# Performance work log

Hardware: AMD Instinct MI355X
Metric: run time of the kernel (lower is better)

Reference implementation:

```python
import jax, jax.numpy as jnp
import numpy as np

B, L, DIM = 2, 2048, 1024
H, DH, W = 16, 64, 256  # heads, head_dim, window_size
ROPE_BASE = 10000.0


def _rope(x):
    # x: [b, l, h, d] -> rotate consecutive pairs (torch view_as_complex semantics)
    l, d = x.shape[1], x.shape[3]
    freqs = 1.0 / (ROPE_BASE ** (jnp.arange(0, d, 2, dtype=jnp.float32) / d))  # [d/2]
    ang = jnp.arange(l, dtype=jnp.float32)[:, None] * freqs[None, :]           # [l, d/2]
    cos = jnp.cos(ang)[None, :, None, :].astype(x.dtype)
    sin = jnp.sin(ang)[None, :, None, :].astype(x.dtype)
    xe, xo = x[..., 0::2], x[..., 1::2]
    ye = xe * cos - xo * sin
    yo = xe * sin + xo * cos
    return jnp.stack([ye, yo], axis=-1).reshape(x.shape)


def setup_inputs() -> dict:
    key = jax.random.key(0)
    ks = jax.random.split(key, 7)
    sh = (B, L, DIM)
    return {
        "q": jax.random.normal(ks[0], sh, jnp.float32),
        "k": jax.random.normal(ks[1], sh, jnp.float32),
        "v": jax.random.normal(ks[2], sh, jnp.float32),
        "wq": jax.random.normal(ks[3], (H * DH, DIM), jnp.float32) * 0.02,
        "wk": jax.random.normal(ks[4], (H * DH, DIM), jnp.float32) * 0.02,
        "wv": jax.random.normal(ks[5], (H * DH, DIM), jnp.float32) * 0.02,
        "wo": jax.random.normal(ks[6], (DIM, H * DH), jnp.float32) * 0.02,
    }


def reference(q, k, v, wq, wk, wv, wo):
    b, l, _ = q.shape
    qh = (q @ wq.T).reshape(b, l, H, DH)
    kh = (k @ wk.T).reshape(b, l, H, DH)
    vh = (v @ wv.T).reshape(b, l, H, DH).transpose(0, 2, 1, 3)  # [b,h,l,d]
    qh = _rope(qh).transpose(0, 2, 1, 3)                        # [b,h,l,d]
    kh = _rope(kh).transpose(0, 2, 1, 3)
    scores = jnp.einsum('bhqd,bhkd->bhqk', qh, kh) * (DH ** -0.5)
    i = jnp.arange(l)[:, None]
    j = jnp.arange(l)[None, :]
    window_mask = (j <= i) & (j >= i - W)  # keys in [i-W, i], matches the loop
    scores = jnp.where(window_mask, scores, -1e30)
    probs = jax.nn.softmax(scores, axis=-1)
    out = jnp.einsum('bhqk,bhkd->bhqd', probs, vh)
    out = out.transpose(0, 2, 1, 3).reshape(b, l, H * DH)
    return out @ wo.T
```

## Files before the change

kernel.cpp:

```cpp
#include <hip/hip_runtime.h>
#include <stdint.h>

#define B_    2
#define L_    2048
#define DIM_  1024
#define H_    16
#define DH_   64
#define WWIN  256

typedef __attribute__((ext_vector_type(4))) float f32x4;
typedef __attribute__((ext_vector_type(8))) short bf16x8;

__device__ __forceinline__ unsigned short f2bf(float x) {
  union { float f; unsigned u; } c; c.f = x;
  unsigned r = c.u + 0x7fffu + ((c.u >> 16) & 1u);
  return (unsigned short)(r >> 16);
}

struct CastArgs {
  const float* src[7];
  unsigned short* dst[7];
  int n[7];
};
__global__ __launch_bounds__(256) void cast_bf16_kernel(CastArgs a) {
  int arr = blockIdx.y;
  int i = (blockIdx.x * 256 + threadIdx.x) * 4;
  if (i >= a.n[arr]) return;
  float4 v = *(const float4*)(a.src[arr] + i);
  ushort4 o;
  o.x = f2bf(v.x); o.y = f2bf(v.y); o.z = f2bf(v.z); o.w = f2bf(v.w);
  *(ushort4*)(a.dst[arr] + i) = o;
}

#define BM 128
#define BN 64
#define BK 64

__device__ __forceinline__ void gld_lds16(const void* g, void* l) {
  __builtin_amdgcn_global_load_lds(
      (const __attribute__((address_space(1))) void*)g,
      (__attribute__((address_space(3))) void*)l, 16, 0, 0);
}

__device__ __forceinline__ void gemm_core_1024(
    const unsigned short* __restrict__ A, const unsigned short* __restrict__ Bt,
    unsigned short* As, unsigned short* Bs, f32x4 (&acc)[2][4],
    int m0, int n0) {
  const int tid = threadIdx.x;
  const int wave = tid >> 6, lane = tid & 63;
  const int quad = lane >> 4, l16 = lane & 15;
  const int srow = tid >> 3, sc = tid & 7;

  auto stage = [&](int k0, int buf) {
    unsigned short* Ad = As + buf * 8192;
    unsigned short* Bd = Bs + buf * 4096;
    #pragma unroll
    for (int rd = 0; rd < 4; ++rd) {
      int row = rd * 32 + srow;
      int cs = sc ^ (row & 7);
      gld_lds16(A + (size_t)(m0 + row) * 1024 + k0 + cs * 8, Ad + row * BK + sc * 8);
    }
    #pragma unroll
    for (int rd = 0; rd < 2; ++rd) {
      int row = rd * 32 + srow;
      int cs = sc ^ (row & 7);
      gld_lds16(Bt + (size_t)(n0 + row) * 1024 + k0 + cs * 8, Bd + row * BK + sc * 8);
    }
  };

  stage(0, 0);
  for (int k = 0; k < 16; ++k) {
    const int cur = k & 1;
    __syncthreads();
    if (k < 15) stage((k + 1) * BK, cur ^ 1);
    const unsigned short* Ac = As + cur * 8192;
    const unsigned short* Bc = Bs + cur * 4096;
    #pragma unroll
    for (int ks = 0; ks < 2; ++ks) {
      bf16x8 af[2], bfr[4];
      #pragma unroll
      for (int i = 0; i < 2; ++i) {
        int row = wave * 32 + i * 16 + l16;
        int ch = (ks * 4 + quad) ^ (row & 7);
        af[i] = *(const bf16x8*)(Ac + row * BK + ch * 8);
      }
      #pragma unroll
      for (int j = 0; j < 4; ++j) {
        int row = j * 16 + l16;
        int ch = (ks * 4 + quad) ^ (row & 7);
        bfr[j] = *(const bf16x8*)(Bc + row * BK + ch * 8);
      }
      #pragma unroll
      for (int i = 0; i < 2; ++i)
        #pragma unroll
        for (int j = 0; j < 4; ++j)
          acc[i][j] = __builtin_amdgcn_mfma_f32_16x16x32_bf16(af[i], bfr[j], acc[i][j], 0, 0, 0);
    }
  }
}

struct ProjArgs {
  const unsigned short* A[3];
  const unsigned short* Bt[3];
  unsigned short* C[3];
};
__global__ __launch_bounds__(256) void gemm_proj_kernel(ProjArgs pa) {
  __shared__ unsigned short SH[24576];
  unsigned short* As = SH;
  unsigned short* Bs = SH + 16384;

  const int bflat = blockIdx.x;
  const int xcd = bflat & 7, s = bflat >> 3;
  const int nblk = s & 15;
  const int mz = xcd * 12 + (s >> 4);
  const int z = mz >> 5;
  const int mblk = mz & 31;
  const int m0 = mblk * BM, n0 = nblk * BN;

  f32x4 acc[2][4] = {};
  gemm_core_1024(pa.A[z], pa.Bt[z], As, Bs, acc, m0, n0);

  const int tid = threadIdx.x;
  const int lane = tid & 63, wave = tid >> 6;
  const int quad = lane >> 4, l16 = lane & 15;

  if (z < 2) {
    float frev[4];
    #pragma unroll
    for (int j = 0; j < 4; ++j) {
      int d = j * 16 + l16;
      frev[j] = exp2f(-(float)(d >> 1) * 0.41524101186092029f) * 0.15915494309189535f;
    }
    unsigned short* C = pa.C[z];
    const int h = nblk;
    const bool even = (l16 & 1) == 0;
    #pragma unroll
    for (int i = 0; i < 2; ++i)
      #pragma unroll
      for (int r = 0; r < 4; ++r) {
        int m = m0 + wave * 32 + i * 16 + quad * 4 + r;
        int b = m >> 11, l = m & (L_ - 1);
        float lf = (float)l;
        #pragma unroll
        for (int j = 0; j < 4; ++j) {
          int d = j * 16 + l16;
          float v = acc[i][j][r];
          float p = __shfl_xor(v, 1);
          float a = lf * frev[j];
          float t = a - floorf(a);
          float sn = __builtin_amdgcn_sinf(t);
          float cs = __builtin_amdgcn_cosf(t);
          float o = even ? (v * cs - p * sn) : (p * sn + v * cs);
          C[(((size_t)b * H_ + h) * L_ + l) * DH_ + d] = f2bf(o);
        }
      }
  } else {
    __syncthreads();
    unsigned short* T = SH + wave * 2304;
    #pragma unroll
    for (int i = 0; i < 2; ++i)
      #pragma unroll
      for (int j = 0; j < 4; ++j) {
        int nw = j * 16 + l16;
        int hm = i * 4 + quad;
        uint2 pk;
        pk.x = (unsigned)f2bf(acc[i][j][0]) | ((unsigned)f2bf(acc[i][j][1]) << 16);
        pk.y = (unsigned)f2bf(acc[i][j][2]) | ((unsigned)f2bf(acc[i][j][3]) << 16);
        *(uint2*)(T + nw * 36 + hm * 4) = pk;
      }
    asm volatile("s_waitcnt lgkmcnt(0)" ::: "memory");
    int h = nblk;
    int d = lane;
    int b = m0 >> 11;
    int lbase = (m0 & (L_ - 1)) + wave * 32;
    unsigned short* C = pa.C[2];
    size_t rowbase = (((size_t)b * H_ + h) * DH_ + d) * L_ + lbase;
    #pragma unroll
    for (int t = 0; t < 4; ++t) {
      uint2 lo = *(uint2*)(T + lane * 36 + t * 8);
      uint2 hi = *(uint2*)(T + lane * 36 + t * 8 + 4);
      uint4 o = {lo.x, lo.y, hi.x, hi.y};
      *(uint4*)(C + rowbase + t * 8) = o;
    }
  }
}

__global__ __launch_bounds__(256) void gemm_out_kernel(
    const unsigned short* __restrict__ A, const unsigned short* __restrict__ Bt,
    float* __restrict__ C) {
  __shared__ unsigned short SH[24576];
  unsigned short* As = SH;
  unsigned short* Bs = SH + 16384;

  const int bflat = blockIdx.x;
  const int xcd = bflat & 7, s = bflat >> 3;
  const int nblk = s & 15;
  const int mblk = xcd * 4 + (s >> 4);
  const int m0 = mblk * BM, n0 = nblk * BN;

  f32x4 acc[2][4] = {};
  gemm_core_1024(A, Bt, As, Bs, acc, m0, n0);

  const int lane = threadIdx.x & 63, wave = threadIdx.x >> 6;
  const int quad = lane >> 4, l16 = lane & 15;
  #pragma unroll
  for (int i = 0; i < 2; ++i)
    #pragma unroll
    for (int j = 0; j < 4; ++j)
      #pragma unroll
      for (int r = 0; r < 4; ++r) {
        int m = m0 + wave * 32 + i * 16 + quad * 4 + r;
        int n = n0 + j * 16 + l16;
        C[(size_t)m * DIM_ + n] = acc[i][j][r];
      }
}

#define NCH 20
__global__ __launch_bounds__(256) void attn_kernel(
    const unsigned short* __restrict__ Qh,
    const unsigned short* __restrict__ Kh,
    const unsigned short* __restrict__ Vt,
    unsigned short* __restrict__ O) {
  __shared__ unsigned short KVs[160 * 72];
  __shared__ unsigned short Ps[4][16 * 40];
  const int tid = threadIdx.x;
  const int wave = tid >> 6, lane = tid & 63;
  const int quad = lane >> 4, l16 = lane & 15;

  const int bflat = blockIdx.x;
  const int xcd = bflat & 7, s = bflat >> 3;
  const int qt = s >> 2;
  const int bh = xcd * 4 + (s & 3);

  const int q0 = qt * 64;
  const int kwin0 = q0 - WWIN;
  const int qb = q0 + wave * 16;

  bf16x8 qf0, qf1;
  {
    const unsigned short* qrow = Qh + ((size_t)bh * L_ + qb + l16) * DH_;
    qf0 = *(const bf16x8*)(qrow + quad * 8);
    qf1 = *(const bf16x8*)(qrow + 32 + quad * 8);
  }

  f32x4 S[NCH] = {};

  #pragma unroll
  for (int half = 0; half < 2; ++half) {
    __syncthreads();
    for (int rep = 0; rep < 5; ++rep) {
      int ci = rep * 256 + tid;
      int row = ci >> 3, c = ci & 7;
      int key = kwin0 + half * 160 + row;
      uint4 val = {0, 0, 0, 0};
      if (key >= 0)
        val = *(const uint4*)(Kh + ((size_t)bh * L_ + key) * DH_ + c * 8);
      *(uint4*)(&KVs[row * 72 + c * 8]) = val;
    }
    __syncthreads();
    #pragma unroll
    for (int cc = 0; cc < 10; ++cc) {
      const unsigned short* kr = &KVs[(cc * 16 + l16) * 72];
      bf16x8 kf0 = *(const bf16x8*)(kr + quad * 8);
      bf16x8 kf1 = *(const bf16x8*)(kr + 32 + quad * 8);
      int c = half * 10 + cc;
      S[c] = __builtin_amdgcn_mfma_f32_16x16x32_bf16(qf0, kf0, S[c], 0, 0, 0);
      S[c] = __builtin_amdgcn_mfma_f32_16x16x32_bf16(qf1, kf1, S[c], 0, 0, 0);
    }
  }

  float inv_l[4];
  #pragma unroll
  for (int r = 0; r < 4; ++r) {
    int i = qb + quad * 4 + r;
    float mx = -1e30f;
    #pragma unroll
    for (int c = 0; c < NCH; ++c) {
      int key = kwin0 + c * 16 + l16;
      bool valid = (key >= 0) && (key <= i) && (key >= i - WWIN);
      float v = valid ? S[c][r] * 0.125f : -1e30f;
      S[c][r] = v;
      mx = fmaxf(mx, v);
    }
    mx = fmaxf(mx, __shfl_xor(mx, 1));
    mx = fmaxf(mx, __shfl_xor(mx, 2));
    mx = fmaxf(mx, __shfl_xor(mx, 4));
    mx = fmaxf(mx, __shfl_xor(mx, 8));
    float sum = 0.f;
    #pragma unroll
    for (int c = 0; c < NCH; ++c) {
      float e = __expf(S[c][r] - mx);
      S[c][r] = e;
      sum += e;
    }
    sum += __shfl_xor(sum, 1);
    sum += __shfl_xor(sum, 2);
    sum += __shfl_xor(sum, 4);
    sum += __shfl_xor(sum, 8);
    inv_l[r] = 1.0f / sum;
  }

  f32x4 Oacc[4] = {};
  #pragma unroll
  for (int half = 0; half < 2; ++half) {
    __syncthreads();
    for (int rep = 0; rep < 5; ++rep) {
      int ci = rep * 256 + tid;
      int row = ci / 20, c = ci % 20;
      int key0 = kwin0 + half * 160 + c * 8;
      uint4 val = {0, 0, 0, 0};
      if (key0 >= 0)
        val = *(const uint4*)(Vt + ((size_t)bh * DH_ + row) * L_ + key0);
      *(uint4*)(&KVs[row * 168 + c * 8]) = val;
    }
    __syncthreads();
    #pragma unroll
    for (int s5 = 0; s5 < 5; ++s5) {
      int cbase = half * 10 + s5 * 2;
      unsigned short* pw = &Ps[wave][0];
      #pragma unroll
      for (int cc = 0; cc < 2; ++cc)
        #pragma unroll
        for (int r = 0; r < 4; ++r) {
          float p = S[cbase + cc][r] * inv_l[r];
          pw[(quad * 4 + r) * 40 + cc * 16 + l16] = f2bf(p);
        }
      asm volatile("s_waitcnt lgkmcnt(0)" ::: "memory");
      bf16x8 pf = *(const bf16x8*)(pw + l16 * 40 + quad * 8);
      int lk = s5 * 32 + quad * 8;
      #pragma unroll
      for (int t = 0; t < 4; ++t) {
        bf16x8 vf = *(const bf16x8*)(&KVs[(t * 16 + l16) * 168 + lk]);
        Oacc[t] = __builtin_amdgcn_mfma_f32_16x16x32_bf16(pf, vf, Oacc[t], 0, 0, 0);
      }
    }
  }

  int b = bh >> 4, h = bh & 15;
  #pragma unroll
  for (int t = 0; t < 4; ++t)
    #pragma unroll
    for (int r = 0; r < 4; ++r) {
      int l = qb + quad * 4 + r;
      int col = h * DH_ + t * 16 + l16;
      O[((size_t)b * L_ + l) * (H_ * DH_) + col] = f2bf(Oacc[t][r]);
    }
}

extern "C" void kernel_launch(void* const* d_in, const int* in_sizes, int n_in,
                              void* d_out, int out_size, void* d_ws, size_t ws_size,
                              hipStream_t stream) {
  const float* q  = (const float*)d_in[0];
  const float* k  = (const float*)d_in[1];
  const float* v  = (const float*)d_in[2];
  const float* wq = (const float*)d_in[3];
  const float* wk = (const float*)d_in[4];
  const float* wv = (const float*)d_in[5];
  const float* wo = (const float*)d_in[6];

  const size_t SA = (size_t)B_ * L_ * DIM_;
  const size_t SW = (size_t)DIM_ * DIM_;
  unsigned short* w   = (unsigned short*)d_ws;
  unsigned short* qb  = w; w += SA;
  unsigned short* kb  = w; w += SA;
  unsigned short* vb  = w; w += SA;
  unsigned short* wqb = w; w += SW;
  unsigned short* wkb = w; w += SW;
  unsigned short* wvb = w; w += SW;
  unsigned short* wob = w; w += SW;
  unsigned short* qh  = w; w += SA;
  unsigned short* kh  = w; w += SA;
  unsigned short* vt  = w; w += SA;
  unsigned short* Ob  = w; w += SA;

  CastArgs ca;
  ca.src[0] = q;  ca.dst[0] = qb;  ca.n[0] = (int)SA;
  ca.src[1] = k;  ca.dst[1] = kb;  ca.n[1] = (int)SA;
  ca.src[2] = v;  ca.dst[2] = vb;  ca.n[2] = (int)SA;
  ca.src[3] = wq; ca.dst[3] = wqb; ca.n[3] = (int)SW;
  ca.src[4] = wk; ca.dst[4] = wkb; ca.n[4] = (int)SW;
  ca.src[5] = wv; ca.dst[5] = wvb; ca.n[5] = (int)SW;
  ca.src[6] = wo; ca.dst[6] = wob; ca.n[6] = (int)SW;
  cast_bf16_kernel<<<dim3(SA / (256 * 4), 7), 256, 0, stream>>>(ca);

  ProjArgs pa;
  pa.A[0] = qb; pa.Bt[0] = wqb; pa.C[0] = qh;
  pa.A[1] = kb; pa.Bt[1] = wkb; pa.C[1] = kh;
  pa.A[2] = vb; pa.Bt[2] = wvb; pa.C[2] = vt;
  gemm_proj_kernel<<<dim3(16 * 32 * 3), 256, 0, stream>>>(pa);

  attn_kernel<<<dim3(32 * 32), 256, 0, stream>>>(qh, kh, vt, Ob);
  gemm_out_kernel<<<dim3(16 * 32), 256, 0, stream>>>(Ob, wob, (float*)d_out);
}
```

Baseline: 190.8 us.

## Split attention into single-wave blocks loading K/V directly from global

The attention kernel changes from 256-thread blocks covering 64 queries to 64-thread blocks covering 16 queries, and the grid grows fourfold. K and V fragments are read straight from global memory into registers instead of being staged through shared memory with block barriers. The key window shrinks to the 17 chunks a 16-query tile needs. The aim is to remove barrier and LDS staging costs and to raise parallelism, at the cost of more redundant global reads of K/V across neighbouring blocks and uncoalesced per-lane loads.

```diff
diff --git a/kernel.cpp b/kernel.cpp
--- a/kernel.cpp
+++ b/kernel.cpp
@@ -215,16 +215,14 @@
       }
 }
 
-#define NCH 20
-__global__ __launch_bounds__(256) void attn_kernel(
+#define NCH 17
+__global__ __launch_bounds__(64) void attn_kernel(
     const unsigned short* __restrict__ Qh,
     const unsigned short* __restrict__ Kh,
     const unsigned short* __restrict__ Vt,
     unsigned short* __restrict__ O) {
-  __shared__ unsigned short KVs[160 * 72];
-  __shared__ unsigned short Ps[4][16 * 40];
-  const int tid = threadIdx.x;
-  const int wave = tid >> 6, lane = tid & 63;
+  __shared__ unsigned short Ps[16 * 296];
+  const int lane = threadIdx.x;
   const int quad = lane >> 4, l16 = lane & 15;
 
   const int bflat = blockIdx.x;
@@ -232,47 +230,35 @@
   const int qt = s >> 2;
   const int bh = xcd * 4 + (s & 3);
 
-  const int q0 = qt * 64;
+  const int q0 = qt * 16;
   const int kwin0 = q0 - WWIN;
-  const int qb = q0 + wave * 16;
+
+  const unsigned short* Kbase = Kh + (size_t)bh * L_ * DH_;
+  const unsigned short* Vbase = Vt + (size_t)bh * DH_ * L_;
 
   bf16x8 qf0, qf1;
   {
-    const unsigned short* qrow = Qh + ((size_t)bh * L_ + qb + l16) * DH_;
+    const unsigned short* qrow = Qh + ((size_t)bh * L_ + q0 + l16) * DH_;
     qf0 = *(const bf16x8*)(qrow + quad * 8);
     qf1 = *(const bf16x8*)(qrow + 32 + quad * 8);
   }
 
   f32x4 S[NCH] = {};
-
-  #pragma unroll
-  for (int half = 0; half < 2; ++half) {
-    __syncthreads();
-    for (int rep = 0; rep < 5; ++rep) {
-      int ci = rep * 256 + tid;
-      int row = ci >> 3, c = ci & 7;
-      int key = kwin0 + half * 160 + row;
-      uint4 val = {0, 0, 0, 0};
-      if (key >= 0)
-        val = *(const uint4*)(Kh + ((size_t)bh * L_ + key) * DH_ + c * 8);
-      *(uint4*)(&KVs[row * 72 + c * 8]) = val;
-    }
-    __syncthreads();
-    #pragma unroll
-    for (int cc = 0; cc < 10; ++cc) {
-      const unsigned short* kr = &KVs[(cc * 16 + l16) * 72];
-      bf16x8 kf0 = *(const bf16x8*)(kr + quad * 8);
-      bf16x8 kf1 = *(const bf16x8*)(kr + 32 + quad * 8);
-      int c = half * 10 + cc;
-      S[c] = __builtin_amdgcn_mfma_f32_16x16x32_bf16(qf0, kf0, S[c], 0, 0, 0);
-      S[c] = __builtin_amdgcn_mfma_f32_16x16x32_bf16(qf1, kf1, S[c], 0, 0, 0);
-    }
+  #pragma unroll
+  for (int cc = 0; cc < NCH; ++cc) {
+    int key = kwin0 + cc * 16 + l16;
+    key = key < 0 ? 0 : key;
+    const unsigned short* kr = Kbase + (size_t)key * DH_;
+    bf16x8 kf0 = *(const bf16x8*)(kr + quad * 8);
+    bf16x8 kf1 = *(const bf16x8*)(kr + 32 + quad * 8);
+    S[cc] = __builtin_amdgcn_mfma_f32_16x16x32_bf16(qf0, kf0, S[cc], 0, 0, 0);
+    S[cc] = __builtin_amdgcn_mfma_f32_16x16x32_bf16(qf1, kf1, S[cc], 0, 0, 0);
   }
 
   float inv_l[4];
   #pragma unroll
   for (int r = 0; r < 4; ++r) {
-    int i = qb + quad * 4 + r;
+    int i = q0 + quad * 4 + r;
     float mx = -1e30f;
     #pragma unroll
     for (int c = 0; c < NCH; ++c) {
@@ -300,39 +286,27 @@
     inv_l[r] = 1.0f / sum;
   }
 
+  #pragma unroll
+  for (int cc = 0; cc < NCH; ++cc)
+    #pragma unroll
+    for (int r = 0; r < 4; ++r)
+      Ps[(quad * 4 + r) * 296 + cc * 16 + l16] = f2bf(S[cc][r] * inv_l[r]);
+  #pragma unroll
+  for (int r = 0; r < 4; ++r)
+    Ps[(quad * 4 + r) * 296 + 272 + l16] = 0;
+  asm volatile("s_waitcnt lgkmcnt(0)" ::: "memory");
+
   f32x4 Oacc[4] = {};
   #pragma unroll
-  for (int half = 0; half < 2; ++half) {
-    __syncthreads();
-    for (int rep = 0; rep < 5; ++rep) {
-      int ci = rep * 256 + tid;
-      int row = ci / 20, c = ci % 20;
-      int key0 = kwin0 + half * 160 + c * 8;
-      uint4 val = {0, 0, 0, 0};
-      if (key0 >= 0)
-        val = *(const uint4*)(Vt + ((size_t)bh * DH_ + row) * L_ + key0);
-      *(uint4*)(&KVs[row * 168 + c * 8]) = val;
-    }
-    __syncthreads();
-    #pragma unroll
-    for (int s5 = 0; s5 < 5; ++s5) {
-      int cbase = half * 10 + s5 * 2;
-      unsigned short* pw = &Ps[wave][0];
-      #pragma unroll
-      for (int cc = 0; cc < 2; ++cc)
-        #pragma unroll
-        for (int r = 0; r < 4; ++r) {
-          float p = S[cbase + cc][r] * inv_l[r];
-          pw[(quad * 4 + r) * 40 + cc * 16 + l16] = f2bf(p);
-        }
-      asm volatile("s_waitcnt lgkmcnt(0)" ::: "memory");
-      bf16x8 pf = *(const bf16x8*)(pw + l16 * 40 + quad * 8);
-      int lk = s5 * 32 + quad * 8;
-      #pragma unroll
-      for (int t = 0; t < 4; ++t) {
-        bf16x8 vf = *(const bf16x8*)(&KVs[(t * 16 + l16) * 168 + lk]);
-        Oacc[t] = __builtin_amdgcn_mfma_f32_16x16x32_bf16(pf, vf, Oacc[t], 0, 0, 0);
-      }
+  for (int g = 0; g < 9; ++g) {
+    bf16x8 pf = *(const bf16x8*)(&Ps[l16 * 296 + g * 32 + quad * 8]);
+    int kk = kwin0 + g * 32 + quad * 8;
+    kk = kk < 0 ? 0 : kk;
+    kk = kk > (L_ - 8) ? (L_ - 8) : kk;
+    #pragma unroll
+    for (int t = 0; t < 4; ++t) {
+      bf16x8 vf = *(const bf16x8*)(Vbase + (size_t)(t * 16 + l16) * L_ + kk);
+      Oacc[t] = __builtin_amdgcn_mfma_f32_16x16x32_bf16(pf, vf, Oacc[t], 0, 0, 0);
     }
   }
 
@@ -341,7 +315,7 @@
   for (int t = 0; t < 4; ++t)
     #pragma unroll
     for (int r = 0; r < 4; ++r) {
-      int l = qb + quad * 4 + r;
+      int l = q0 + quad * 4 + r;
       int col = h * DH_ + t * 16 + l16;
       O[((size_t)b * L_ + l) * (H_ * DH_) + col] = f2bf(Oacc[t][r]);
     }
@@ -389,6 +363,6 @@
   pa.A[2] = vb; pa.Bt[2] = wvb; pa.C[2] = vt;
   gemm_proj_kernel<<<dim3(16 * 32 * 3), 256, 0, stream>>>(pa);
 
-  attn_kernel<<<dim3(32 * 32), 256, 0, stream>>>(qh, kh, vt, Ob);
+  attn_kernel<<<dim3(128 * 32), 64, 0, stream>>>(qh, kh, vt, Ob);
   gemm_out_kernel<<<dim3(16 * 32), 256, 0, stream>>>(Ob, wob, (float*)d_out);
 }
```

After: 197.6 us. 1.04x slower.
